# Performance work log

Hardware: AMD Instinct MI355X
Metric: run time of the kernel (lower is better)

The kernel has to match this reference:

```python
import jax, jax.numpy as jnp
import numpy as np

B, C, N, K = 4, 256, 8192, 16
H, S = 8, 2            # num_heads, num_scale
HC = C // H            # head_channels = 32
CS = C // S            # per-scale channels = 128
HS = H // S            # heads per scale = 4
KV_CH = (64, 128)
EPS = 1e-5
SCALE = HC ** -0.5


def setup_inputs() -> dict:
    key = jax.random.key(0)
    ks = jax.random.split(key, 20)
    d = {}
    d["x"] = jax.random.normal(ks[0], (B, C, N), jnp.float32)
    d["y0"] = jax.random.normal(ks[1], (B, KV_CH[0], N, K), jnp.float32)
    d["y1"] = jax.random.normal(ks[2], (B, KV_CH[1], N, K), jnp.float32)
    d["q_w"] = jax.random.normal(ks[3], (C, C), jnp.float32) * 0.02
    for i, c in enumerate(KV_CH):
        kk = jax.random.split(ks[4 + i], 4)
        d[f"conv{i}_w"] = jax.random.normal(kk[0], (CS, c), jnp.float32) * 0.05  # 1x1 conv
        d[f"bn{i}_g"] = jnp.ones((CS,), jnp.float32)
        d[f"bn{i}_b"] = jnp.zeros((CS,), jnp.float32)
        d[f"bn{i}_m"] = jax.random.normal(kk[1], (CS,), jnp.float32) * 0.1
        d[f"bn{i}_v"] = jax.random.uniform(kk[2], (CS,), jnp.float32) + 0.5
        d[f"kv{i}_w"] = jax.random.normal(kk[3], (2 * CS, CS), jnp.float32) * 0.02
    d["proj_w"] = jax.random.normal(ks[8], (C, C), jnp.float32) * 0.02
    d["proj_b"] = jnp.zeros((C,), jnp.float32)
    return d


def _scale_branch(q_i, y, conv_w, g, b, m, v, kv_w):
    # q_i: [B, HS, N, HC];  y: [B, c, N, K]
    z = jnp.einsum('bcnk,oc->bonk', y, conv_w)                 # 1x1 conv -> [B, CS, N, K]
    inv = (g / jnp.sqrt(v + EPS))[None, :, None, None]
    z = jax.nn.relu((z - m[None, :, None, None]) * inv + b[None, :, None, None])
    kv = jnp.transpose(z, (0, 2, 3, 1)) @ kv_w.T               # [B, N, K, 2*CS]
    kv = kv.reshape(B, N, K, HS, HC, 2)
    k = jnp.transpose(kv[..., 0], (0, 3, 1, 2, 4))             # [B, HS, N, K, HC]
    vv = jnp.transpose(kv[..., 1], (0, 3, 1, 2, 4))            # [B, HS, N, K, HC]
    attn = jax.nn.softmax(jnp.einsum('bhnd,bhnkd->bhnk', q_i, k) * SCALE, axis=-1)
    out = jnp.einsum('bhnk,bhnkd->bhnd', attn, vv)             # [B, HS, N, HC]
    return jnp.transpose(out, (0, 2, 1, 3)).reshape(B, N, HS * HC)


def reference(x, y0, y1, q_w,
              conv0_w, bn0_g, bn0_b, bn0_m, bn0_v, kv0_w,
              conv1_w, bn1_g, bn1_b, bn1_m, bn1_v, kv1_w,
              proj_w, proj_b):
    xt = jnp.swapaxes(x, 1, 2)                                 # [B, N, C]
    q = (xt @ q_w.T).reshape(B, N, H, HC).transpose(0, 2, 1, 3)  # [B, H, N, HC]
    o0 = _scale_branch(q[:, :HS], y0, conv0_w, bn0_g, bn0_b, bn0_m, bn0_v, kv0_w)
    o1 = _scale_branch(q[:, HS:], y1, conv1_w, bn1_g, bn1_b, bn1_m, bn1_v, kv1_w)
    outs = jnp.concatenate([o0, o1], axis=-1)                  # [B, N, C]
    outs = outs @ proj_w.T + proj_b
    return jnp.swapaxes(outs, 1, 2)                            # [B, C, N]
```

## Files before the change

### kernel.cpp

```cpp
#include <hip/hip_runtime.h>

typedef __attribute__((ext_vector_type(8))) short bf16x8;
typedef __attribute__((ext_vector_type(4))) float f32x4;
typedef unsigned short ushort_t;
typedef unsigned int uint_t;

#define MFMA(a, b, c) __builtin_amdgcn_mfma_f32_16x16x32_bf16(a, b, c, 0, 0, 0)

namespace {
constexpr int Bn = 4;
constexpr int Nn = 8192;
constexpr float SCALEf = 0.17677669529663687f;
constexpr float EPSf = 1e-5f;

constexpr size_t WS_QW  = 0;
constexpr size_t WS_PW  = 131072;
constexpr size_t WS_KW0 = 262144;
constexpr size_t WS_KW1 = 327680;
constexpr size_t WS_CW0 = 393216;
constexpr size_t WS_CW1 = 409600;
constexpr size_t WS_CB0 = 442368;
constexpr size_t WS_CB1 = 442880;
constexpr size_t WS_AO  = 458752;
}

__device__ __forceinline__ uint_t f2b(float f) {
    union { float f; uint_t u; } v; v.f = f;
    return (v.u + 0x7fffu + ((v.u >> 16) & 1u)) >> 16;
}
__device__ __forceinline__ float b2f(ushort_t u) {
    union { uint_t u; float f; } v; v.u = ((uint_t)u) << 16;
    return v.f;
}

template<int KC>
__device__ __forceinline__ int swz(int r, int c) {
    constexpr int SW = (KC / 8 < 16 ? KC / 8 : 16);
    return r * KC + ((((c >> 3) ^ (r & (SW - 1))) << 3) | (c & 7));
}

__global__ void plsa_prep(const float* __restrict__ qw,
                          const float* __restrict__ c0w, const float* __restrict__ g0,
                          const float* __restrict__ b0,  const float* __restrict__ m0,
                          const float* __restrict__ v0,  const float* __restrict__ k0w,
                          const float* __restrict__ c1w, const float* __restrict__ g1,
                          const float* __restrict__ b1,  const float* __restrict__ m1,
                          const float* __restrict__ v1,  const float* __restrict__ k1w,
                          const float* __restrict__ pw,  char* ws) {
    const int i = blockIdx.x * 256 + threadIdx.x;
    ((ushort_t*)(ws + WS_QW))[i] = (ushort_t)f2b(qw[i]);
    ((ushort_t*)(ws + WS_PW))[i] = (ushort_t)f2b(pw[i]);
    if (i < 32768) {
        ((ushort_t*)(ws + WS_KW0))[i] = (ushort_t)f2b(k0w[i]);
        ((ushort_t*)(ws + WS_KW1))[i] = (ushort_t)f2b(k1w[i]);
    }
    if (i < 8192)  { int o = i >> 6;  float inv = g0[o] * rsqrtf(v0[o] + EPSf);
                     ((ushort_t*)(ws + WS_CW0))[i] = (ushort_t)f2b(c0w[i] * inv); }
    if (i < 16384) { int o = i >> 7;  float inv = g1[o] * rsqrtf(v1[o] + EPSf);
                     ((ushort_t*)(ws + WS_CW1))[i] = (ushort_t)f2b(c1w[i] * inv); }
    if (i < 128) {
        float i0 = g0[i] * rsqrtf(v0[i] + EPSf);
        float i1 = g1[i] * rsqrtf(v1[i] + EPSf);
        ((float*)(ws + WS_CB0))[i] = b0[i] - m0[i] * i0;
        ((float*)(ws + WS_CB1))[i] = b1[i] - m1[i] * i1;
    }
}

template<int CIN>
__device__ __forceinline__ void issue_y2(const float* __restrict__ yb, int b, int n0c,
                                         float* yreg, int tid) {
    constexpr int ITER = CIN / 16;
    #pragma unroll
    for (int it = 0; it < ITER; ++it) {
        const int idx = tid + it * 256;
        const int pk = idx & 31, c0 = (idx >> 5) * 2;
        const float* ysrc = yb + ((size_t)(b * CIN + c0)) * (Nn * 16)
                               + (size_t)(n0c + (pk >> 4)) * 16 + (pk & 15);
        yreg[it * 2]     = ysrc[0];
        yreg[it * 2 + 1] = ysrc[(size_t)Nn * 16];
    }
}
template<int CIN>
__device__ __forceinline__ void write_y2(ushort_t* Ys, const float* yreg, int tid) {
    constexpr int ITER = CIN / 16;
    #pragma unroll
    for (int it = 0; it < ITER; ++it) {
        const int idx = tid + it * 256;
        const int pk = idx & 31, c0 = (idx >> 5) * 2;
        *(uint_t*)(Ys + swz<CIN>(pk, c0)) = f2b(yreg[it * 2]) | (f2b(yreg[it * 2 + 1]) << 16);
    }
}

template<int CIN, int NCIN>
__device__ __forceinline__ void branch_run(
    int tid, int b, int n0,
    const float* __restrict__ yb, const float* __restrict__ ynext,
    const char* __restrict__ ws,
    ushort_t* Ys, ushort_t* Zs, ushort_t* Ks, ushort_t* Vs,
    const ushort_t* qs, ushort_t* aobuf, float* yreg)
{
    constexpr size_t wcw = (CIN == 64) ? WS_CW0 : WS_CW1;
    constexpr size_t wcb = (CIN == 64) ? WS_CB0 : WS_CB1;
    constexpr size_t wkw = (CIN == 64) ? WS_KW0 : WS_KW1;
    constexpr int qb = (CIN == 64) ? 0 : 128;
    constexpr int KT = CIN / 32;

    const ushort_t* cwb = (const ushort_t*)(ws + wcw);
    const float*    cbb = (const float*)(ws + wcb);
    const ushort_t* kwb = (const ushort_t*)(ws + wkw);
    const int w = tid >> 6, lane = tid & 63, l15 = lane & 15, lk = lane >> 4;

    #pragma unroll 1
    for (int cc = 0; cc < 8; ++cc) {
        if (cc < 7) issue_y2<CIN>(yb, b, n0 + (cc + 1) * 2, yreg, tid);
        else if constexpr (NCIN != 0) issue_y2<NCIN>(ynext, b, n0, yreg, tid);

        #pragma unroll
        for (int ct = 0; ct < 2; ++ct) {
            bf16x8 bfr[KT];
            #pragma unroll
            for (int k = 0; k < KT; ++k)
                bfr[k] = *(const bf16x8*)(Ys + swz<CIN>(ct * 16 + l15, k * 32 + lk * 8));
            #pragma unroll
            for (int mi = 0; mi < 2; ++mi) {
                f32x4 a = f32x4{0.f, 0.f, 0.f, 0.f};
                #pragma unroll
                for (int k = 0; k < KT; ++k) {
                    bf16x8 af = *(const bf16x8*)(cwb + ((w * 2 + mi) * 16 + l15) * CIN + k * 32 + lk * 8);
                    a = MFMA(af, bfr[k], a);
                }
                const int col = ct * 16 + l15, o0 = (w * 2 + mi) * 16 + lk * 4;
                const float4 cb4 = *(const float4*)(cbb + (w * 2 + mi) * 16 + lk * 4);
                const float z0 = fmaxf(a.x + cb4.x, 0.f);
                const float z1 = fmaxf(a.y + cb4.y, 0.f);
                const float z2 = fmaxf(a.z + cb4.z, 0.f);
                const float z3 = fmaxf(a.w + cb4.w, 0.f);
                const int off = swz<128>(col, o0);
                *(uint_t*)(Zs + off)     = f2b(z0) | (f2b(z1) << 16);
                *(uint_t*)(Zs + off + 2) = f2b(z2) | (f2b(z3) << 16);
            }
        }
        __syncthreads();

        #pragma unroll
        for (int ct = 0; ct < 2; ++ct) {
            bf16x8 bfr[4];
            #pragma unroll
            for (int k = 0; k < 4; ++k)
                bfr[k] = *(const bf16x8*)(Zs + swz<128>(ct * 16 + l15, k * 32 + lk * 8));
            const int col = ct * 16 + l15;
            #pragma unroll
            for (int mi = 0; mi < 4; ++mi) {
                f32x4 a = f32x4{0.f, 0.f, 0.f, 0.f};
                #pragma unroll
                for (int k = 0; k < 4; ++k) {
                    bf16x8 af = *(const bf16x8*)(kwb + ((w * 4 + mi) * 16 + l15) * 128 + k * 32 + lk * 8);
                    a = MFMA(af, bfr[k], a);
                }
                const int j0 = (w * 4 + mi) * 16 + lk * 4;
                const int h = j0 >> 6;
                const int d0 = (j0 & 63) >> 1;
                *(uint_t*)(Ks + swz<128>(col, h * 32 + d0)) = f2b(a.x) | (f2b(a.z) << 16);
                Vs[swz<32>(h * 32 + d0,     col)] = (ushort_t)f2b(a.y);
                Vs[swz<32>(h * 32 + d0 + 1, col)] = (ushort_t)f2b(a.w);
            }
        }
        if (cc < 7) write_y2<CIN>(Ys, yreg, tid);
        else if constexpr (NCIN != 0) write_y2<NCIN>(Ys, yreg, tid);
        __syncthreads();

        {
            const int pt = w >> 1, pr = w & 1;
            float p = 0.f;
            if (lane < 32) {
                const int kk = lane & 15;
                const int h = pr * 2 + (lane >> 4);
                float s = 0.f;
                #pragma unroll
                for (int dc = 0; dc < 4; ++dc) {
                    bf16x8 q8 = *(const bf16x8*)(qs + swz<256>(cc * 2 + pt, qb + h * 32 + dc * 8));
                    bf16x8 k8 = *(const bf16x8*)(Ks + swz<128>(pt * 16 + kk, h * 32 + dc * 8));
                    #pragma unroll
                    for (int j = 0; j < 8; ++j)
                        s += b2f((ushort_t)q8[j]) * b2f((ushort_t)k8[j]);
                }
                s *= SCALEf;
                float mx = s;
                #pragma unroll
                for (int m = 1; m < 16; m <<= 1) mx = fmaxf(mx, __shfl_xor(mx, m));
                const float e = __expf(s - mx);
                float sum = e;
                #pragma unroll
                for (int m = 1; m < 16; m <<= 1) sum += __shfl_xor(sum, m);
                p = e / sum;
            }
            const int d = lane & 31, hh2 = lane >> 5;
            const int h2 = pr * 2 + hh2;
            const int row = h2 * 32 + d;
            bf16x8 va = *(const bf16x8*)(Vs + swz<32>(row, pt * 16));
            bf16x8 vb = *(const bf16x8*)(Vs + swz<32>(row, pt * 16 + 8));
            float o = 0.f;
            #pragma unroll
            for (int j = 0; j < 8; ++j) {
                o += __shfl(p, hh2 * 16 + j)     * b2f((ushort_t)va[j]);
                o += __shfl(p, hh2 * 16 + 8 + j) * b2f((ushort_t)vb[j]);
            }
            aobuf[((size_t)(b * Nn + n0 + cc * 2 + pt)) * 256 + qb + h2 * 32 + d] = (ushort_t)f2b(o);
        }
    }
}

__global__ __launch_bounds__(256, 2) void k_attn(
    const float* __restrict__ x, const float* __restrict__ y0, const float* __restrict__ y1,
    const char* __restrict__ ws, ushort_t* __restrict__ aobuf) {

    __shared__ __align__(16) ushort_t qs[4096];
    __shared__ __align__(16) ushort_t Ys[4096];
    __shared__ __align__(16) ushort_t Zs[4096];
    __shared__ __align__(16) ushort_t Ks[4096];
    __shared__ __align__(16) ushort_t Vs[4096];

    const int tid = threadIdx.x;
    const int b = blockIdx.x >> 9, n0 = (blockIdx.x & 511) << 4;
    const int w = tid >> 6, lane = tid & 63, l15 = lane & 15, lk = lane >> 4;
    float yreg[16];

    const int xn = tid & 15, cg = tid >> 4;
    #pragma unroll
    for (int hseg = 0; hseg < 2; ++hseg) {
        float xreg[8];
        #pragma unroll
        for (int i = 0; i < 8; ++i)
            xreg[i] = x[((size_t)(b * 256 + cg * 16 + hseg * 8 + i)) * Nn + n0 + xn];
        #pragma unroll
        for (int j = 0; j < 4; ++j)
            *(uint_t*)(Ys + swz<256>(xn, cg * 16 + hseg * 8 + 2 * j)) =
                f2b(xreg[2 * j]) | (f2b(xreg[2 * j + 1]) << 16);
    }
    issue_y2<64>(y0, b, n0, yreg, tid);
    __syncthreads();

    {
        const ushort_t* qwb = (const ushort_t*)(ws + WS_QW);
        #pragma unroll
        for (int mi = 0; mi < 4; ++mi) {
            f32x4 acc = f32x4{0.f, 0.f, 0.f, 0.f};
            #pragma unroll
            for (int k = 0; k < 8; ++k) {
                bf16x8 af = *(const bf16x8*)(qwb + ((w * 4 + mi) * 16 + l15) * 256 + k * 32 + lk * 8);
                bf16x8 bf = *(const bf16x8*)(Ys + swz<256>(l15, k * 32 + lk * 8));
                acc = MFMA(af, bf, acc);
            }
            const int ch0 = (w * 4 + mi) * 16 + lk * 4;
            uint2 u;
            u.x = f2b(acc.x) | (f2b(acc.y) << 16);
            u.y = f2b(acc.z) | (f2b(acc.w) << 16);
            *(uint2*)(qs + swz<256>(l15, ch0)) = u;
        }
    }
    __syncthreads();

    write_y2<64>(Ys, yreg, tid);
    __syncthreads();

    branch_run<64, 128>(tid, b, n0, y0, y1, ws, Ys, Zs, Ks, Vs, qs, aobuf, yreg);
    branch_run<128, 0> (tid, b, n0, y1, nullptr, ws, Ys, Zs, Ks, Vs, qs, aobuf, yreg);
}

__global__ __launch_bounds__(256, 2) void k_proj(const char* __restrict__ ws,
                                                 const float* __restrict__ proj_b,
                                                 float* __restrict__ out) {
    __shared__ __align__(16) ushort_t At[64 * 256];
    const ushort_t* pwb = (const ushort_t*)(ws + WS_PW);
    const ushort_t* aobuf = (const ushort_t*)(ws + WS_AO);
    const int tid = threadIdx.x;
    const int b = blockIdx.x >> 7, n0 = (blockIdx.x & 127) * 64;

    {
        const int cp = tid & 127, ng = tid >> 7;
        #pragma unroll
        for (int i = 0; i < 32; ++i) {
            const int n = ng + i * 2;
            const uint_t u = *(const uint_t*)(aobuf + ((size_t)(b * Nn + n0 + n)) * 256 + cp * 2);
            *(uint_t*)(At + swz<256>(n, cp * 2)) = u;
        }
    }
    __syncthreads();

    const int w = tid >> 6, lane = tid & 63, l15 = lane & 15, lk = lane >> 4;
    #pragma unroll
    for (int mi = 0; mi < 4; ++mi) {
        bf16x8 af[8];
        #pragma unroll
        for (int k = 0; k < 8; ++k)
            af[k] = *(const bf16x8*)(pwb + (w * 64 + mi * 16 + l15) * 256 + k * 32 + lk * 8);
        const int ch0 = w * 64 + mi * 16 + lk * 4;
        const float4 pbv = *(const float4*)(proj_b + ch0);
        #pragma unroll
        for (int ct = 0; ct < 4; ++ct) {
            f32x4 acc = f32x4{0.f, 0.f, 0.f, 0.f};
            #pragma unroll
            for (int k = 0; k < 8; ++k) {
                bf16x8 bf = *(const bf16x8*)(At + swz<256>(ct * 16 + l15, k * 32 + lk * 8));
                acc = MFMA(af[k], bf, acc);
            }
            const int nn = n0 + ct * 16 + l15;
            out[((size_t)(b * 256 + ch0 + 0)) * Nn + nn] = acc.x + pbv.x;
            out[((size_t)(b * 256 + ch0 + 1)) * Nn + nn] = acc.y + pbv.y;
            out[((size_t)(b * 256 + ch0 + 2)) * Nn + nn] = acc.z + pbv.z;
            out[((size_t)(b * 256 + ch0 + 3)) * Nn + nn] = acc.w + pbv.w;
        }
    }
}

extern "C" void kernel_launch(void* const* d_in, const int* in_sizes, int n_in,
                              void* d_out, int out_size, void* d_ws, size_t ws_size,
                              hipStream_t stream) {
    const float* x       = (const float*)d_in[0];
    const float* y0      = (const float*)d_in[1];
    const float* y1      = (const float*)d_in[2];
    const float* q_w     = (const float*)d_in[3];
    const float* conv0_w = (const float*)d_in[4];
    const float* bn0_g   = (const float*)d_in[5];
    const float* bn0_b   = (const float*)d_in[6];
    const float* bn0_m   = (const float*)d_in[7];
    const float* bn0_v   = (const float*)d_in[8];
    const float* kv0_w   = (const float*)d_in[9];
    const float* conv1_w = (const float*)d_in[10];
    const float* bn1_g   = (const float*)d_in[11];
    const float* bn1_b   = (const float*)d_in[12];
    const float* bn1_m   = (const float*)d_in[13];
    const float* bn1_v   = (const float*)d_in[14];
    const float* kv1_w   = (const float*)d_in[15];
    const float* proj_w  = (const float*)d_in[16];
    const float* proj_b  = (const float*)d_in[17];
    char* ws = (char*)d_ws;

    plsa_prep<<<256, 256, 0, stream>>>(q_w, conv0_w, bn0_g, bn0_b, bn0_m, bn0_v, kv0_w,
                                       conv1_w, bn1_g, bn1_b, bn1_m, bn1_v, kv1_w,
                                       proj_w, ws);
    k_attn<<<Bn * (Nn / 16), 256, 0, stream>>>(x, y0, y1, ws,
                                               (ushort_t*)(ws + WS_AO));
    k_proj<<<Bn * (Nn / 64), 256, 0, stream>>>(ws, proj_b, (float*)d_out);
}
```

Baseline: 278.3 us.

## Fuse output projection into attention kernel via shared-memory staging

The attention kernel now writes its per-tile attention output (16 points × 256 channels, bf16) into a new shared-memory buffer instead of a global workspace. After both scale branches it runs the output projection GEMM itself and writes the fp32 result with bias directly. This removes the separate projection kernel launch and the global round-trip of the intermediate attention output. In exchange it adds 8 KB of LDS per block, which may lower occupancy. The projection weights are also re-read per 16-point tile rather than per 64-point tile.

Result: slower. 288.8 us (+3.8%).

```diff
diff --git a/kernel.cpp b/kernel.cpp
--- a/kernel.cpp
+++ b/kernel.cpp
@@ -21,7 +21,6 @@
 constexpr size_t WS_CW1 = 409600;
 constexpr size_t WS_CB0 = 442368;
 constexpr size_t WS_CB1 = 442880;
-constexpr size_t WS_AO  = 458752;
 }
 
 __device__ __forceinline__ uint_t f2b(float f) {
@@ -97,7 +96,7 @@
     const float* __restrict__ yb, const float* __restrict__ ynext,
     const char* __restrict__ ws,
     ushort_t* Ys, ushort_t* Zs, ushort_t* Ks, ushort_t* Vs,
-    const ushort_t* qs, ushort_t* aobuf, float* yreg)
+    const ushort_t* qs, ushort_t* Atl, float* yreg)
 {
     constexpr size_t wcw = (CIN == 64) ? WS_CW0 : WS_CW1;
     constexpr size_t wcb = (CIN == 64) ? WS_CB0 : WS_CB1;
@@ -205,16 +204,18 @@
                 o += __shfl(p, hh2 * 16 + j)     * b2f((ushort_t)va[j]);
                 o += __shfl(p, hh2 * 16 + 8 + j) * b2f((ushort_t)vb[j]);
             }
-            aobuf[((size_t)(b * Nn + n0 + cc * 2 + pt)) * 256 + qb + h2 * 32 + d] = (ushort_t)f2b(o);
+            Atl[swz<256>(cc * 2 + pt, qb + h2 * 32 + d)] = (ushort_t)f2b(o);
         }
     }
 }
 
 __global__ __launch_bounds__(256, 2) void k_attn(
     const float* __restrict__ x, const float* __restrict__ y0, const float* __restrict__ y1,
-    const char* __restrict__ ws, ushort_t* __restrict__ aobuf) {
+    const char* __restrict__ ws, const float* __restrict__ proj_b,
+    float* __restrict__ out) {
 
     __shared__ __align__(16) ushort_t qs[4096];
+    __shared__ __align__(16) ushort_t Atl[4096];
     __shared__ __align__(16) ushort_t Ys[4096];
     __shared__ __align__(16) ushort_t Zs[4096];
     __shared__ __align__(16) ushort_t Ks[4096];
@@ -263,48 +264,24 @@
     write_y2<64>(Ys, yreg, tid);
     __syncthreads();
 
-    branch_run<64, 128>(tid, b, n0, y0, y1, ws, Ys, Zs, Ks, Vs, qs, aobuf, yreg);
-    branch_run<128, 0> (tid, b, n0, y1, nullptr, ws, Ys, Zs, Ks, Vs, qs, aobuf, yreg);
-}
-
-__global__ __launch_bounds__(256, 2) void k_proj(const char* __restrict__ ws,
-                                                 const float* __restrict__ proj_b,
-                                                 float* __restrict__ out) {
-    __shared__ __align__(16) ushort_t At[64 * 256];
-    const ushort_t* pwb = (const ushort_t*)(ws + WS_PW);
-    const ushort_t* aobuf = (const ushort_t*)(ws + WS_AO);
-    const int tid = threadIdx.x;
-    const int b = blockIdx.x >> 7, n0 = (blockIdx.x & 127) * 64;
+    branch_run<64, 128>(tid, b, n0, y0, y1, ws, Ys, Zs, Ks, Vs, qs, Atl, yreg);
+    branch_run<128, 0> (tid, b, n0, y1, nullptr, ws, Ys, Zs, Ks, Vs, qs, Atl, yreg);
+    __syncthreads();
 
     {
-        const int cp = tid & 127, ng = tid >> 7;
-        #pragma unroll
-        for (int i = 0; i < 32; ++i) {
-            const int n = ng + i * 2;
-            const uint_t u = *(const uint_t*)(aobuf + ((size_t)(b * Nn + n0 + n)) * 256 + cp * 2);
-            *(uint_t*)(At + swz<256>(n, cp * 2)) = u;
-        }
-    }
-    __syncthreads();
-
-    const int w = tid >> 6, lane = tid & 63, l15 = lane & 15, lk = lane >> 4;
-    #pragma unroll
-    for (int mi = 0; mi < 4; ++mi) {
-        bf16x8 af[8];
-        #pragma unroll
-        for (int k = 0; k < 8; ++k)
-            af[k] = *(const bf16x8*)(pwb + (w * 64 + mi * 16 + l15) * 256 + k * 32 + lk * 8);
-        const int ch0 = w * 64 + mi * 16 + lk * 4;
-        const float4 pbv = *(const float4*)(proj_b + ch0);
-        #pragma unroll
-        for (int ct = 0; ct < 4; ++ct) {
+        const ushort_t* pwb = (const ushort_t*)(ws + WS_PW);
+        #pragma unroll
+        for (int mi = 0; mi < 4; ++mi) {
             f32x4 acc = f32x4{0.f, 0.f, 0.f, 0.f};
             #pragma unroll
             for (int k = 0; k < 8; ++k) {
-                bf16x8 bf = *(const bf16x8*)(At + swz<256>(ct * 16 + l15, k * 32 + lk * 8));
-                acc = MFMA(af[k], bf, acc);
-            }
-            const int nn = n0 + ct * 16 + l15;
+                bf16x8 af = *(const bf16x8*)(pwb + ((w * 4 + mi) * 16 + l15) * 256 + k * 32 + lk * 8);
+                bf16x8 bf = *(const bf16x8*)(Atl + swz<256>(l15, k * 32 + lk * 8));
+                acc = MFMA(af, bf, acc);
+            }
+            const int ch0 = (w * 4 + mi) * 16 + lk * 4;
+            const float4 pbv = *(const float4*)(proj_b + ch0);
+            const int nn = n0 + l15;
             out[((size_t)(b * 256 + ch0 + 0)) * Nn + nn] = acc.x + pbv.x;
             out[((size_t)(b * 256 + ch0 + 1)) * Nn + nn] = acc.y + pbv.y;
             out[((size_t)(b * 256 + ch0 + 2)) * Nn + nn] = acc.z + pbv.z;
@@ -339,7 +316,5 @@
     plsa_prep<<<256, 256, 0, stream>>>(q_w, conv0_w, bn0_g, bn0_b, bn0_m, bn0_v, kv0_w,
                                        conv1_w, bn1_g, bn1_b, bn1_m, bn1_v, kv1_w,
                                        proj_w, ws);
-    k_attn<<<Bn * (Nn / 16), 256, 0, stream>>>(x, y0, y1, ws,
-                                               (ushort_t*)(ws + WS_AO));
-    k_proj<<<Bn * (Nn / 64), 256, 0, stream>>>(ws, proj_b, (float*)d_out);
-}
+    k_attn<<<Bn * (Nn / 16), 256, 0, stream>>>(x, y0, y1, ws, proj_b, (float*)d_out);
+}
```
